# Optimization experiments

Measured on AMD Instinct MI355X. Metric: run time of the kernel, lower is better.

Reference implementation:

```python
import jax, jax.numpy as jnp
import numpy as np

N_NODES = 50000
N_EDGES = 800000
IN_F = 128
HID = 16
HEADS = 8
OUT_F = 128


def setup_inputs() -> dict:
    key = jax.random.key(0)
    ks = jax.random.split(key, 16)
    h = jax.random.normal(ks[0], (N_NODES, IN_F), dtype=jnp.float32)
    src1 = jax.random.randint(ks[1], (N_EDGES,), 0, N_NODES, dtype=jnp.int32)
    dst1 = jax.random.randint(ks[2], (N_EDGES,), 0, N_NODES, dtype=jnp.int32)
    src2 = jax.random.randint(ks[3], (N_EDGES,), 0, N_NODES, dtype=jnp.int32)
    dst2 = jax.random.randint(ks[4], (N_EDGES,), 0, N_NODES, dtype=jnp.int32)
    norm1 = jax.random.uniform(ks[5], (N_NODES, 1), dtype=jnp.float32)
    norm2 = jax.random.uniform(ks[6], (N_NODES, 1), dtype=jnp.float32)
    D = HEADS * HID  # 128
    W_lin = jax.random.normal(ks[7], (IN_F, D), dtype=jnp.float32) * (1.0 / np.sqrt(IN_F))
    b_lin = jax.random.normal(ks[8], (D,), dtype=jnp.float32) * 0.01
    al = jax.random.normal(ks[9], (HEADS, HID, 1), dtype=jnp.float32) * 0.1
    ar = jax.random.normal(ks[10], (HEADS, HID, 1), dtype=jnp.float32) * 0.1
    W_fc = jax.random.normal(ks[11], (D, OUT_F), dtype=jnp.float32) * (1.0 / np.sqrt(D))
    b_fc = jax.random.normal(ks[12], (OUT_F,), dtype=jnp.float32) * 0.01
    return {"h": h, "src1": src1, "dst1": dst1, "src2": src2, "dst2": dst2,
            "norm1": norm1, "norm2": norm2, "W_lin": W_lin, "b_lin": b_lin,
            "al": al, "ar": ar, "W_fc": W_fc, "b_fc": b_fc}


def _propagate(feat, norm, src, dst, n_nodes):
    # msg = h[src] * norm[src]; accum[v] = sum_{e: dst=v} msg_e; out = accum * norm
    msg = feat[src] * norm[src]                      # [E, D]
    agg = jax.ops.segment_sum(msg, dst, num_segments=n_nodes)
    return agg * norm                                # [N, D]


def _leaky_relu(x):
    return jnp.where(x > 0, x, 0.2 * x)


def reference(h, src1, dst1, src2, dst2, norm1, norm2, W_lin, b_lin, al, ar, W_fc, b_fc):
    N = h.shape[0]
    hf = h @ W_lin + b_lin                           # [N, 8*HID] (dropout p given but eval-mode -> identity)
    h1 = _propagate(hf, norm1, src1, dst1, N)
    h2 = _propagate(hf, norm2, src2, dst2, N)
    # Faithful to torch: row-major reshape [N, 8*HID] -> (8, N, HID)
    h1r = h1.reshape(HEADS, N, HID)
    h2r = h2.reshape(HEADS, N, HID)
    hr = hf.reshape(HEADS, N, HID)
    ai = jnp.einsum('hnd,hdo->hno', hr, al)          # [8, N, 1]
    aj1 = jnp.einsum('hnd,hdo->hno', h1r, ar)
    aj2 = jnp.einsum('hnd,hdo->hno', h2r, ar)
    a1 = jnp.clip(jnp.exp(_leaky_relu(ai + aj1)), -10.0, 10.0)
    a2 = jnp.clip(jnp.exp(_leaky_relu(ai + aj2)), -10.0, 10.0)
    denom = a1 + a2
    out = (a1 / denom) * h1r + (a2 / denom) * h2r    # [8, N, HID]
    out = out.reshape(N, HEADS * HID)
    return out @ W_fc + b_fc
```

## Files before the change

### kernel.cpp

```cpp
#include <hip/hip_runtime.h>

#define NN 50000
#define NE 800000
#define NB 196
#define NBLK 128
#define CHUNK 6250
#define MAXB 6144

typedef __bf16 bf16x8 __attribute__((ext_vector_type(8)));
typedef float  f32x4  __attribute__((ext_vector_type(4)));

__device__ __forceinline__ unsigned short f2bf(float x) {
    unsigned u = __float_as_uint(x);
    return (unsigned short)((u + 0x7FFFu + ((u >> 16) & 1u)) >> 16);
}
__device__ __forceinline__ float bflo(unsigned u) { return __uint_as_float(u << 16); }
__device__ __forceinline__ float bfhi(unsigned u) { return __uint_as_float(u & 0xFFFF0000u); }

__global__ __launch_bounds__(256) void convert_w_kernel(
    const float* __restrict__ Wa, const float* __restrict__ Wb,
    unsigned short* __restrict__ Wta, unsigned short* __restrict__ Wtb)
{
    __shared__ float ls[128 * 132];
    const float* W = blockIdx.x ? Wb : Wa;
    unsigned short* Wt = blockIdx.x ? Wtb : Wta;
    const int t = threadIdx.x;
    for (int i = t; i < 128 * 32; i += 256) {
        int k = i >> 5, n4 = i & 31;
        *(float4*)&ls[k * 132 + n4 * 4] = ((const float4*)W)[i];
    }
    __syncthreads();
    for (int j = t; j < 128 * 128; j += 256) {
        int n = j >> 7, k = j & 127;
        Wt[j] = f2bf(ls[k * 132 + n]);
    }
}

__global__ __launch_bounds__(256) void mfma_gemm_kernel(
    const float* __restrict__ X, const unsigned short* __restrict__ Wt,
    const float* __restrict__ bias, float* __restrict__ Y,
    unsigned short* __restrict__ Ybf, int nrows)
{
    __shared__ unsigned short Wl[128 * 128];
    const int t = threadIdx.x;
    const int lane = t & 63;
    const int wv = t >> 6;
    const int row0 = blockIdx.x * 64;
    const int m16 = lane & 15;
    const int quad = lane >> 4;

    {
        const uint4* Wg = (const uint4*)Wt;
        #pragma unroll
        for (int i = 0; i < 8; i++) {
            int gi = t + i * 256;
            int n = gi >> 4, g = gi & 15;
            uint4 v = Wg[gi];
            *(uint4*)&Wl[n * 128 + (((g ^ (n & 15)) << 3))] = v;
        }
    }

    const int arow = row0 + wv * 16 + m16;
    const bool valid = (arow < nrows);
    const float4* X4 = (const float4*)X;
    float4 xr[8];
    #pragma unroll
    for (int kc = 0; kc < 4; kc++) {
        if (valid) {
            int gidx = arow * 32 + kc * 8 + quad * 2;
            xr[kc * 2]     = X4[gidx];
            xr[kc * 2 + 1] = X4[gidx + 1];
        } else {
            xr[kc * 2] = xr[kc * 2 + 1] = make_float4(0.f, 0.f, 0.f, 0.f);
        }
    }
    __syncthreads();

    f32x4 acc[8];
    #pragma unroll
    for (int nt = 0; nt < 8; nt++) acc[nt] = (f32x4){0.f, 0.f, 0.f, 0.f};

    #pragma unroll
    for (int kc = 0; kc < 4; kc++) {
        union { unsigned short u[8]; bf16x8 v; } ah, al;
        float f[8] = { xr[kc*2].x, xr[kc*2].y, xr[kc*2].z, xr[kc*2].w,
                       xr[kc*2+1].x, xr[kc*2+1].y, xr[kc*2+1].z, xr[kc*2+1].w };
        #pragma unroll
        for (int j = 0; j < 8; j++) {
            unsigned u = __float_as_uint(f[j]);
            ah.u[j] = (unsigned short)(u >> 16);
            al.u[j] = f2bf(f[j] - __uint_as_float(u & 0xFFFF0000u));
        }
        const int sgbase = (kc * 4 + quad);
        #pragma unroll
        for (int nt = 0; nt < 8; nt++) {
            const int n = nt * 16 + m16;
            bf16x8 b = *(const bf16x8*)&Wl[n * 128 + ((sgbase ^ m16) << 3)];
            acc[nt] = __builtin_amdgcn_mfma_f32_16x16x32_bf16(ah.v, b, acc[nt], 0, 0, 0);
            acc[nt] = __builtin_amdgcn_mfma_f32_16x16x32_bf16(al.v, b, acc[nt], 0, 0, 0);
        }
    }

    #pragma unroll
    for (int nt = 0; nt < 8; nt++) {
        const int col = nt * 16 + m16;
        const float bc = bias[col];
        #pragma unroll
        for (int r = 0; r < 4; r++) {
            int row = row0 + wv * 16 + quad * 4 + r;
            if (row < nrows) {
                float val = acc[nt][r] + bc;
                if (Y)   Y[(long)row * 128 + col] = val;
                if (Ybf) Ybf[(long)row * 128 + col] = f2bf(val);
            }
        }
    }
}

__global__ __launch_bounds__(256) void mfma_gemm_bf16_kernel(
    const unsigned short* __restrict__ Xbf, const unsigned short* __restrict__ Wt,
    const float* __restrict__ bias, float* __restrict__ Y, int nrows)
{
    __shared__ unsigned short Wl[128 * 128];
    const int t = threadIdx.x;
    const int lane = t & 63;
    const int wv = t >> 6;
    const int row0 = blockIdx.x * 64;
    const int m16 = lane & 15;
    const int quad = lane >> 4;

    {
        const uint4* Wg = (const uint4*)Wt;
        #pragma unroll
        for (int i = 0; i < 8; i++) {
            int gi = t + i * 256;
            int n = gi >> 4, g = gi & 15;
            uint4 v = Wg[gi];
            *(uint4*)&Wl[n * 128 + (((g ^ (n & 15)) << 3))] = v;
        }
    }

    const int arow = row0 + wv * 16 + m16;
    const bool valid = (arow < nrows);
    const uint4* X16 = (const uint4*)Xbf;
    union { uint4 u; bf16x8 v; } xr[4];
    #pragma unroll
    for (int kc = 0; kc < 4; kc++) {
        if (valid) xr[kc].u = X16[arow * 16 + kc * 4 + quad];
        else       xr[kc].u = make_uint4(0, 0, 0, 0);
    }
    __syncthreads();

    f32x4 acc[8];
    #pragma unroll
    for (int nt = 0; nt < 8; nt++) acc[nt] = (f32x4){0.f, 0.f, 0.f, 0.f};

    #pragma unroll
    for (int kc = 0; kc < 4; kc++) {
        const int sgbase = (kc * 4 + quad);
        #pragma unroll
        for (int nt = 0; nt < 8; nt++) {
            const int n = nt * 16 + m16;
            bf16x8 b = *(const bf16x8*)&Wl[n * 128 + ((sgbase ^ m16) << 3)];
            acc[nt] = __builtin_amdgcn_mfma_f32_16x16x32_bf16(xr[kc].v, b, acc[nt], 0, 0, 0);
        }
    }

    #pragma unroll
    for (int nt = 0; nt < 8; nt++) {
        const int col = nt * 16 + m16;
        const float bc = bias[col];
        #pragma unroll
        for (int r = 0; r < 4; r++) {
            int row = row0 + wv * 16 + quad * 4 + r;
            if (row < nrows) Y[(long)row * 128 + col] = acc[nt][r] + bc;
        }
    }
}

__global__ __launch_bounds__(1024) void histA_kernel(
    const int* __restrict__ dst1, const int* __restrict__ dst2, int* __restrict__ histG)
{
    __shared__ int h[2 * NB];
    const int t = threadIdx.x, blk = blockIdx.x;
    for (int i = t; i < 2 * NB; i += 1024) h[i] = 0;
    __syncthreads();
    const int base = blk * CHUNK;
    for (int i = t; i < CHUNK; i += 1024) {
        atomicAdd(&h[dst1[base + i] >> 8], 1);
        atomicAdd(&h[NB + (dst2[base + i] >> 8)], 1);
    }
    __syncthreads();
    for (int i = t; i < 2 * NB; i += 1024)
        histG[(size_t)i * NBLK + blk] = h[i];
}

__global__ __launch_bounds__(NBLK) void scanB1_kernel(int* __restrict__ histG, int* __restrict__ btot)
{
    __shared__ int s[NBLK];
    const int t = threadIdx.x, row = blockIdx.x;
    int v = histG[(size_t)row * NBLK + t];
    s[t] = v;
    __syncthreads();
    for (int off = 1; off < NBLK; off <<= 1) {
        int x = (t >= off) ? s[t - off] : 0;
        __syncthreads();
        s[t] += x;
        __syncthreads();
    }
    histG[(size_t)row * NBLK + t] = s[t] - v;
    if (t == NBLK - 1) btot[row] = s[t];
}

__global__ __launch_bounds__(256) void scanB2_kernel(const int* __restrict__ btot, int* __restrict__ bbase)
{
    __shared__ int sc[256];
    const int t = threadIdx.x;
    for (int g = 0; g < 2; g++) {
        int v = (t < NB) ? btot[g * NB + t] : 0;
        sc[t] = v;
        __syncthreads();
        for (int off = 1; off < 256; off <<= 1) {
            int x = (t >= off) ? sc[t - off] : 0;
            __syncthreads();
            sc[t] += x;
            __syncthreads();
        }
        if (t < NB) bbase[g * NB + t] = sc[t] - v;
        __syncthreads();
    }
}

__global__ __launch_bounds__(1024) void scatterC_kernel(
    const int* __restrict__ src1, const int* __restrict__ dst1,
    const int* __restrict__ src2, const int* __restrict__ dst2,
    const int* __restrict__ histG, const int* __restrict__ bbase,
    unsigned int* __restrict__ bin1, unsigned int* __restrict__ bin2)
{
    __shared__ int pos[2 * NB];
    const int t = threadIdx.x, blk = blockIdx.x;
    for (int i = t; i < 2 * NB; i += 1024)
        pos[i] = bbase[i] + histG[(size_t)i * NBLK + blk];
    __syncthreads();
    const int base = blk * CHUNK;
    for (int i = t; i < CHUNK; i += 1024) {
        int d = dst1[base + i], s = src1[base + i];
        int slot = atomicAdd(&pos[d >> 8], 1);
        bin1[slot] = ((unsigned)(d & 255) << 16) | (unsigned)s;
        d = dst2[base + i]; s = src2[base + i];
        slot = atomicAdd(&pos[NB + (d >> 8)], 1);
        bin2[slot] = ((unsigned)(d & 255) << 16) | (unsigned)s;
    }
}

__global__ __launch_bounds__(256) void bucket_sort_kernel(
    const unsigned int* __restrict__ bin1, const unsigned int* __restrict__ bin2,
    const int* __restrict__ bbase, const int* __restrict__ btot,
    unsigned short* __restrict__ csr1, int* __restrict__ start1, int* __restrict__ deg1,
    unsigned short* __restrict__ csr2, int* __restrict__ start2, int* __restrict__ deg2)
{
    __shared__ int lcnt[256];
    __shared__ int sc[256];
    __shared__ int oat[256];
    __shared__ unsigned short outb[MAXB];
    const int t = threadIdx.x;
    const int g = (blockIdx.x >= NB) ? 1 : 0;
    const int b = blockIdx.x - g * NB;
    const unsigned int* bin = g ? bin2 : bin1;
    unsigned short* csr = g ? csr2 : csr1;
    int* start = g ? start2 : start1;
    int* deg   = g ? deg2 : deg1;

    const int base = bbase[g * NB + b];
    const int tot = min(btot[g * NB + b], MAXB);

    lcnt[t] = 0;
    __syncthreads();
    for (int i = t; i < tot; i += 256) atomicAdd(&lcnt[bin[base + i] >> 16], 1);
    __syncthreads();
    sc[t] = lcnt[t];
    __syncthreads();
    for (int off = 1; off < 256; off <<= 1) {
        int x = (t >= off) ? sc[t - off] : 0;
        __syncthreads();
        sc[t] += x;
        __syncthreads();
    }
    const int ex = sc[t] - lcnt[t];
    oat[t] = ex;
    __syncthreads();
    for (int i = t; i < tot; i += 256) {
        unsigned v = bin[base + i];
        int slot = atomicAdd(&oat[v >> 16], 1);
        outb[slot] = (unsigned short)(v & 0xFFFFu);
    }
    __syncthreads();
    for (int i = t; i < tot; i += 256) csr[base + i] = outb[i];
    int nd = b * 256 + t;
    if (nd < NN) { start[nd] = base + ex; deg[nd] = lcnt[t]; }
}

__global__ __launch_bounds__(256) void gather_attn_kernel(
    const unsigned int* __restrict__ hfb,
    const unsigned short* __restrict__ csr1, const int* __restrict__ start1,
    const int* __restrict__ deg1, const float* __restrict__ norm1,
    const unsigned short* __restrict__ csr2, const int* __restrict__ start2,
    const int* __restrict__ deg2, const float* __restrict__ norm2,
    const float* __restrict__ al, const float* __restrict__ ar,
    unsigned int* __restrict__ outb)
{
    const int lane = threadIdx.x & 63;
    int node = (blockIdx.x * 256 + threadIdx.x) >> 6;
    if (node >= NN) return;
    node = __builtin_amdgcn_readfirstlane(node);

    float2 acc1 = make_float2(0.f, 0.f), acc2 = make_float2(0.f, 0.f);

    #pragma unroll 1
    for (int g = 0; g < 2; g++) {
        const unsigned short* csr = g ? csr2 : csr1;
        const int* startp = g ? start2 : start1;
        const int* degp   = g ? deg2 : deg1;
        const float* norm = g ? norm2 : norm1;
        float2 acc = make_float2(0.f, 0.f);
        const int st = startp[node], dg = degp[node];
        for (int base = 0; base < dg; base += 64) {
            const int nb = min(64, dg - base);
            int myc = (lane < nb) ? (int)csr[st + base + lane] : 0;
            int j = 0;
            for (; j + 8 <= nb; j += 8) {
                int s[8]; float n[8]; unsigned u[8];
                #pragma unroll
                for (int q = 0; q < 8; q++) s[q] = __builtin_amdgcn_readlane(myc, j + q);
                #pragma unroll
                for (int q = 0; q < 8; q++) {
                    n[q] = norm[s[q]];
                    u[q] = hfb[(long)s[q] * 64 + lane];
                }
                #pragma unroll
                for (int q = 0; q < 8; q++) {
                    acc.x = fmaf(bflo(u[q]), n[q], acc.x);
                    acc.y = fmaf(bfhi(u[q]), n[q], acc.y);
                }
            }
            for (; j < nb; j++) {
                int s = __builtin_amdgcn_readlane(myc, j);
                float nv = norm[s];
                unsigned u = hfb[(long)s * 64 + lane];
                acc.x = fmaf(bflo(u), nv, acc.x);
                acc.y = fmaf(bfhi(u), nv, acc.y);
            }
        }
        if (g) acc2 = acc; else acc1 = acc;
    }

    const float nn1 = norm1[node], nn2 = norm2[node];
    acc1.x *= nn1; acc1.y *= nn1;
    acc2.x *= nn2; acc2.y *= nn2;

    const int cc = lane >> 3;
    const int m = node * 8 + cc;
    const int head = m / NN;
    const int hid = (2 * lane) & 15;
    unsigned uf = hfb[(long)node * 64 + lane];
    const float fx = bflo(uf), fy = bfhi(uf);
    const float av0 = al[head * 16 + hid], av1 = al[head * 16 + hid + 1];
    const float rv0 = ar[head * 16 + hid], rv1 = ar[head * 16 + hid + 1];
    float s_ai = fx * av0 + fy * av1;
    float s1 = acc1.x * rv0 + acc1.y * rv1;
    float s2 = acc2.x * rv0 + acc2.y * rv1;
    s_ai += __shfl_xor(s_ai, 1); s_ai += __shfl_xor(s_ai, 2); s_ai += __shfl_xor(s_ai, 4);
    s1   += __shfl_xor(s1, 1);   s1   += __shfl_xor(s1, 2);   s1   += __shfl_xor(s1, 4);
    s2   += __shfl_xor(s2, 1);   s2   += __shfl_xor(s2, 2);   s2   += __shfl_xor(s2, 4);
    float x1 = s_ai + s1; x1 = x1 > 0.f ? x1 : 0.2f * x1;
    float x2 = s_ai + s2; x2 = x2 > 0.f ? x2 : 0.2f * x2;
    float e1 = fminf(expf(x1), 10.f);
    float e2 = fminf(expf(x2), 10.f);
    float inv = 1.f / (e1 + e2);
    float w1 = e1 * inv, w2 = e2 * inv;
    float ox = w1 * acc1.x + w2 * acc2.x;
    float oy = w1 * acc1.y + w2 * acc2.y;
    outb[(long)node * 64 + lane] = (unsigned)f2bf(ox) | ((unsigned)f2bf(oy) << 16);
}

extern "C" void kernel_launch(void* const* d_in, const int* in_sizes, int n_in,
                              void* d_out, int out_size, void* d_ws, size_t ws_size,
                              hipStream_t stream)
{
    const float* h     = (const float*)d_in[0];
    const int*   src1  = (const int*)  d_in[1];
    const int*   dst1  = (const int*)  d_in[2];
    const int*   src2  = (const int*)  d_in[3];
    const int*   dst2  = (const int*)  d_in[4];
    const float* norm1 = (const float*)d_in[5];
    const float* norm2 = (const float*)d_in[6];
    const float* W_lin = (const float*)d_in[7];
    const float* b_lin = (const float*)d_in[8];
    const float* al    = (const float*)d_in[9];
    const float* ar    = (const float*)d_in[10];
    const float* W_fc  = (const float*)d_in[11];
    const float* b_fc  = (const float*)d_in[12];
    float* out = (float*)d_out;

    unsigned short* hfb  = (unsigned short*)d_ws;
    unsigned short* outbf = hfb + (size_t)NN * 128;
    unsigned int* bin1 = (unsigned int*)(outbf + (size_t)NN * 128);
    unsigned int* bin2 = bin1 + NE;
    unsigned short* csr1 = (unsigned short*)(bin2 + NE);
    unsigned short* csr2 = csr1 + NE;
    unsigned short* WtL  = csr2 + NE;
    unsigned short* WtF  = WtL + 128 * 128;
    int* histG  = (int*)(WtF + 128 * 128);
    int* btot   = histG + 2 * NB * NBLK;
    int* bbase  = btot + 2 * NB;
    int* start1 = bbase + 2 * NB;
    int* start2 = start1 + NN;
    int* deg1   = start2 + NN;
    int* deg2   = deg1 + NN;

    convert_w_kernel<<<2, 256, 0, stream>>>(W_lin, W_fc, WtL, WtF);

    mfma_gemm_kernel<<<(NN + 63) / 64, 256, 0, stream>>>(h, WtL, b_lin, nullptr, hfb, NN);

    histA_kernel<<<NBLK, 1024, 0, stream>>>(dst1, dst2, histG);
    scanB1_kernel<<<2 * NB, NBLK, 0, stream>>>(histG, btot);
    scanB2_kernel<<<1, 256, 0, stream>>>(btot, bbase);
    scatterC_kernel<<<NBLK, 1024, 0, stream>>>(src1, dst1, src2, dst2, histG, bbase, bin1, bin2);
    bucket_sort_kernel<<<2 * NB, 256, 0, stream>>>(bin1, bin2, bbase, btot,
                                                   csr1, start1, deg1,
                                                   csr2, start2, deg2);

    gather_attn_kernel<<<(NN * 64 + 255) / 256, 256, 0, stream>>>(
        (const unsigned int*)hfb,
        csr1, start1, deg1, norm1,
        csr2, start2, deg2, norm2,
        al, ar, (unsigned int*)outbf);

    mfma_gemm_bf16_kernel<<<(NN + 63) / 64, 256, 0, stream>>>(outbf, WtF, b_fc, out, NN);
}
```

Measured before the change: 227.7 us.

## Fuse CSR build into one cooperative kernel and gather two edges per wave

Merges weight conversion, histogram, the two scans, the scatter and the bucket sort into a single cooperative kernel of 512 blocks separated by grid syncs. This removes five kernel launches and the gaps between them. The gather kernel now processes two edges per wave iteration, each half-wave loading 8 bytes per lane, and combines the halves with a cross-half shuffle. The grid syncs add barrier cost, and the cooperative launch requires all 512 blocks to be resident at once.

```diff
diff --git a/kernel.cpp b/kernel.cpp
--- a/kernel.cpp
+++ b/kernel.cpp
@@ -1,10 +1,13 @@
 #include <hip/hip_runtime.h>
+#include <hip/hip_cooperative_groups.h>
+
+namespace cg = cooperative_groups;
 
 #define NN 50000
 #define NE 800000
 #define NB 196
-#define NBLK 128
-#define CHUNK 6250
+#define NBLK 512
+#define CHUNK 1563
 #define MAXB 6144
 
 typedef __bf16 bf16x8 __attribute__((ext_vector_type(8)));
@@ -17,22 +20,138 @@
 __device__ __forceinline__ float bflo(unsigned u) { return __uint_as_float(u << 16); }
 __device__ __forceinline__ float bfhi(unsigned u) { return __uint_as_float(u & 0xFFFF0000u); }
 
-__global__ __launch_bounds__(256) void convert_w_kernel(
+struct SortSM { int lcnt[256]; int sc[256]; int oat[256]; unsigned short outb[MAXB]; };
+
+__global__ __launch_bounds__(256, 2) void build_kernel(
     const float* __restrict__ Wa, const float* __restrict__ Wb,
-    unsigned short* __restrict__ Wta, unsigned short* __restrict__ Wtb)
+    unsigned short* __restrict__ Wta, unsigned short* __restrict__ Wtb,
+    const int* __restrict__ src1, const int* __restrict__ dst1,
+    const int* __restrict__ src2, const int* __restrict__ dst2,
+    int* __restrict__ histG, int* __restrict__ btot, int* __restrict__ bbase,
+    unsigned int* __restrict__ bin1, unsigned int* __restrict__ bin2,
+    unsigned short* __restrict__ csr1, int* __restrict__ start1, int* __restrict__ deg1,
+    unsigned short* __restrict__ csr2, int* __restrict__ start2, int* __restrict__ deg2)
 {
-    __shared__ float ls[128 * 132];
-    const float* W = blockIdx.x ? Wb : Wa;
-    unsigned short* Wt = blockIdx.x ? Wtb : Wta;
+    __shared__ union {
+        int h[2 * NB];
+        int s[256];
+        int pos[2 * NB];
+        SortSM srt;
+    } sm;
+    cg::grid_group grid = cg::this_grid();
     const int t = threadIdx.x;
-    for (int i = t; i < 128 * 32; i += 256) {
-        int k = i >> 5, n4 = i & 31;
-        *(float4*)&ls[k * 132 + n4 * 4] = ((const float4*)W)[i];
-    }
-    __syncthreads();
-    for (int j = t; j < 128 * 128; j += 256) {
-        int n = j >> 7, k = j & 127;
-        Wt[j] = f2bf(ls[k * 132 + n]);
+    const int blk = blockIdx.x;
+
+    {
+        for (int i = t; i < 2 * NB; i += 256) sm.h[i] = 0;
+        __syncthreads();
+        const int base = blk * CHUNK;
+        const int lim = min(CHUNK, NE - base);
+        for (int i = t; i < lim; i += 256) {
+            atomicAdd(&sm.h[dst1[base + i] >> 8], 1);
+            atomicAdd(&sm.h[NB + (dst2[base + i] >> 8)], 1);
+        }
+        __syncthreads();
+        for (int i = t; i < 2 * NB; i += 256)
+            histG[(size_t)i * NBLK + blk] = sm.h[i];
+        if (blk < 2) {
+            const float* W = blk ? Wb : Wa;
+            unsigned short* Wt = blk ? Wtb : Wta;
+            for (int j = t; j < 128 * 128; j += 256) {
+                int n = j >> 7, k = j & 127;
+                Wt[j] = f2bf(W[k * 128 + n]);
+            }
+        }
+    }
+    grid.sync();
+
+    if (blk < 2 * NB) {
+        int* rowp = histG + (size_t)blk * NBLK;
+        int v0 = rowp[2 * t], v1 = rowp[2 * t + 1];
+        sm.s[t] = v0 + v1;
+        __syncthreads();
+        for (int off = 1; off < 256; off <<= 1) {
+            int x = (t >= off) ? sm.s[t - off] : 0;
+            __syncthreads();
+            sm.s[t] += x;
+            __syncthreads();
+        }
+        int incl = sm.s[t];
+        int e0 = incl - (v0 + v1);
+        rowp[2 * t] = e0;
+        rowp[2 * t + 1] = e0 + v0;
+        if (t == 255) btot[blk] = incl;
+    }
+    grid.sync();
+
+    if (blk == 0) {
+        for (int g = 0; g < 2; g++) {
+            int v = (t < NB) ? btot[g * NB + t] : 0;
+            sm.s[t] = v;
+            __syncthreads();
+            for (int off = 1; off < 256; off <<= 1) {
+                int x = (t >= off) ? sm.s[t - off] : 0;
+                __syncthreads();
+                sm.s[t] += x;
+                __syncthreads();
+            }
+            if (t < NB) bbase[g * NB + t] = sm.s[t] - v;
+            __syncthreads();
+        }
+    }
+    grid.sync();
+
+    {
+        for (int i = t; i < 2 * NB; i += 256)
+            sm.pos[i] = bbase[i] + histG[(size_t)i * NBLK + blk];
+        __syncthreads();
+        const int base = blk * CHUNK;
+        const int lim = min(CHUNK, NE - base);
+        for (int i = t; i < lim; i += 256) {
+            int d = dst1[base + i], s = src1[base + i];
+            int slot = atomicAdd(&sm.pos[d >> 8], 1);
+            bin1[slot] = ((unsigned)(d & 255) << 16) | (unsigned)s;
+            d = dst2[base + i]; s = src2[base + i];
+            slot = atomicAdd(&sm.pos[NB + (d >> 8)], 1);
+            bin2[slot] = ((unsigned)(d & 255) << 16) | (unsigned)s;
+        }
+    }
+    grid.sync();
+
+    if (blk < 2 * NB) {
+        const int g = (blk >= NB) ? 1 : 0;
+        const int b = blk - g * NB;
+        const unsigned int* bin = g ? bin2 : bin1;
+        unsigned short* csr = g ? csr2 : csr1;
+        int* start = g ? start2 : start1;
+        int* deg   = g ? deg2 : deg1;
+        const int base = bbase[g * NB + b];
+        const int tot = min(btot[g * NB + b], MAXB);
+
+        sm.srt.lcnt[t] = 0;
+        __syncthreads();
+        for (int i = t; i < tot; i += 256) atomicAdd(&sm.srt.lcnt[bin[base + i] >> 16], 1);
+        __syncthreads();
+        sm.srt.sc[t] = sm.srt.lcnt[t];
+        __syncthreads();
+        for (int off = 1; off < 256; off <<= 1) {
+            int x = (t >= off) ? sm.srt.sc[t - off] : 0;
+            __syncthreads();
+            sm.srt.sc[t] += x;
+            __syncthreads();
+        }
+        const int ex = sm.srt.sc[t] - sm.srt.lcnt[t];
+        sm.srt.oat[t] = ex;
+        __syncthreads();
+        for (int i = t; i < tot; i += 256) {
+            unsigned v = bin[base + i];
+            int slot = atomicAdd(&sm.srt.oat[v >> 16], 1);
+            sm.srt.outb[slot] = (unsigned short)(v & 0xFFFFu);
+        }
+        __syncthreads();
+        for (int i = t; i < tot; i += 256) csr[base + i] = sm.srt.outb[i];
+        int nd = b * 256 + t;
+        if (nd < NN) { start[nd] = base + ex; deg[nd] = sm.srt.lcnt[t]; }
     }
 }
 
@@ -178,128 +297,6 @@
     }
 }
 
-__global__ __launch_bounds__(1024) void histA_kernel(
-    const int* __restrict__ dst1, const int* __restrict__ dst2, int* __restrict__ histG)
-{
-    __shared__ int h[2 * NB];
-    const int t = threadIdx.x, blk = blockIdx.x;
-    for (int i = t; i < 2 * NB; i += 1024) h[i] = 0;
-    __syncthreads();
-    const int base = blk * CHUNK;
-    for (int i = t; i < CHUNK; i += 1024) {
-        atomicAdd(&h[dst1[base + i] >> 8], 1);
-        atomicAdd(&h[NB + (dst2[base + i] >> 8)], 1);
-    }
-    __syncthreads();
-    for (int i = t; i < 2 * NB; i += 1024)
-        histG[(size_t)i * NBLK + blk] = h[i];
-}
-
-__global__ __launch_bounds__(NBLK) void scanB1_kernel(int* __restrict__ histG, int* __restrict__ btot)
-{
-    __shared__ int s[NBLK];
-    const int t = threadIdx.x, row = blockIdx.x;
-    int v = histG[(size_t)row * NBLK + t];
-    s[t] = v;
-    __syncthreads();
-    for (int off = 1; off < NBLK; off <<= 1) {
-        int x = (t >= off) ? s[t - off] : 0;
-        __syncthreads();
-        s[t] += x;
-        __syncthreads();
-    }
-    histG[(size_t)row * NBLK + t] = s[t] - v;
-    if (t == NBLK - 1) btot[row] = s[t];
-}
-
-__global__ __launch_bounds__(256) void scanB2_kernel(const int* __restrict__ btot, int* __restrict__ bbase)
-{
-    __shared__ int sc[256];
-    const int t = threadIdx.x;
-    for (int g = 0; g < 2; g++) {
-        int v = (t < NB) ? btot[g * NB + t] : 0;
-        sc[t] = v;
-        __syncthreads();
-        for (int off = 1; off < 256; off <<= 1) {
-            int x = (t >= off) ? sc[t - off] : 0;
-            __syncthreads();
-            sc[t] += x;
-            __syncthreads();
-        }
-        if (t < NB) bbase[g * NB + t] = sc[t] - v;
-        __syncthreads();
-    }
-}
-
-__global__ __launch_bounds__(1024) void scatterC_kernel(
-    const int* __restrict__ src1, const int* __restrict__ dst1,
-    const int* __restrict__ src2, const int* __restrict__ dst2,
-    const int* __restrict__ histG, const int* __restrict__ bbase,
-    unsigned int* __restrict__ bin1, unsigned int* __restrict__ bin2)
-{
-    __shared__ int pos[2 * NB];
-    const int t = threadIdx.x, blk = blockIdx.x;
-    for (int i = t; i < 2 * NB; i += 1024)
-        pos[i] = bbase[i] + histG[(size_t)i * NBLK + blk];
-    __syncthreads();
-    const int base = blk * CHUNK;
-    for (int i = t; i < CHUNK; i += 1024) {
-        int d = dst1[base + i], s = src1[base + i];
-        int slot = atomicAdd(&pos[d >> 8], 1);
-        bin1[slot] = ((unsigned)(d & 255) << 16) | (unsigned)s;
-        d = dst2[base + i]; s = src2[base + i];
-        slot = atomicAdd(&pos[NB + (d >> 8)], 1);
-        bin2[slot] = ((unsigned)(d & 255) << 16) | (unsigned)s;
-    }
-}
-
-__global__ __launch_bounds__(256) void bucket_sort_kernel(
-    const unsigned int* __restrict__ bin1, const unsigned int* __restrict__ bin2,
-    const int* __restrict__ bbase, const int* __restrict__ btot,
-    unsigned short* __restrict__ csr1, int* __restrict__ start1, int* __restrict__ deg1,
-    unsigned short* __restrict__ csr2, int* __restrict__ start2, int* __restrict__ deg2)
-{
-    __shared__ int lcnt[256];
-    __shared__ int sc[256];
-    __shared__ int oat[256];
-    __shared__ unsigned short outb[MAXB];
-    const int t = threadIdx.x;
-    const int g = (blockIdx.x >= NB) ? 1 : 0;
-    const int b = blockIdx.x - g * NB;
-    const unsigned int* bin = g ? bin2 : bin1;
-    unsigned short* csr = g ? csr2 : csr1;
-    int* start = g ? start2 : start1;
-    int* deg   = g ? deg2 : deg1;
-
-    const int base = bbase[g * NB + b];
-    const int tot = min(btot[g * NB + b], MAXB);
-
-    lcnt[t] = 0;
-    __syncthreads();
-    for (int i = t; i < tot; i += 256) atomicAdd(&lcnt[bin[base + i] >> 16], 1);
-    __syncthreads();
-    sc[t] = lcnt[t];
-    __syncthreads();
-    for (int off = 1; off < 256; off <<= 1) {
-        int x = (t >= off) ? sc[t - off] : 0;
-        __syncthreads();
-        sc[t] += x;
-        __syncthreads();
-    }
-    const int ex = sc[t] - lcnt[t];
-    oat[t] = ex;
-    __syncthreads();
-    for (int i = t; i < tot; i += 256) {
-        unsigned v = bin[base + i];
-        int slot = atomicAdd(&oat[v >> 16], 1);
-        outb[slot] = (unsigned short)(v & 0xFFFFu);
-    }
-    __syncthreads();
-    for (int i = t; i < tot; i += 256) csr[base + i] = outb[i];
-    int nd = b * 256 + t;
-    if (nd < NN) { start[nd] = base + ex; deg[nd] = lcnt[t]; }
-}
-
 __global__ __launch_bounds__(256) void gather_attn_kernel(
     const unsigned int* __restrict__ hfb,
     const unsigned short* __restrict__ csr1, const int* __restrict__ start1,
@@ -310,11 +307,14 @@
     unsigned int* __restrict__ outb)
 {
     const int lane = threadIdx.x & 63;
+    const int half = lane & 31;
+    const bool hi = (lane & 32) != 0;
     int node = (blockIdx.x * 256 + threadIdx.x) >> 6;
     if (node >= NN) return;
     node = __builtin_amdgcn_readfirstlane(node);
 
-    float2 acc1 = make_float2(0.f, 0.f), acc2 = make_float2(0.f, 0.f);
+    float4 acc1 = make_float4(0.f, 0.f, 0.f, 0.f);
+    float4 acc2 = make_float4(0.f, 0.f, 0.f, 0.f);
 
     #pragma unroll 1
     for (int g = 0; g < 2; g++) {
@@ -322,65 +322,96 @@
         const int* startp = g ? start2 : start1;
         const int* degp   = g ? deg2 : deg1;
         const float* norm = g ? norm2 : norm1;
-        float2 acc = make_float2(0.f, 0.f);
+        float4 acc = make_float4(0.f, 0.f, 0.f, 0.f);
         const int st = startp[node], dg = degp[node];
         for (int base = 0; base < dg; base += 64) {
             const int nb = min(64, dg - base);
             int myc = (lane < nb) ? (int)csr[st + base + lane] : 0;
+            const int npairs = nb >> 1;
             int j = 0;
-            for (; j + 8 <= nb; j += 8) {
-                int s[8]; float n[8]; unsigned u[8];
+            for (; j + 4 <= npairs; j += 4) {
+                float fn[4]; uint2 u[4];
                 #pragma unroll
-                for (int q = 0; q < 8; q++) s[q] = __builtin_amdgcn_readlane(myc, j + q);
-                #pragma unroll
-                for (int q = 0; q < 8; q++) {
-                    n[q] = norm[s[q]];
-                    u[q] = hfb[(long)s[q] * 64 + lane];
+                for (int p = 0; p < 4; p++) {
+                    int e = (j + p) * 2;
+                    int s0 = __builtin_amdgcn_readlane(myc, e);
+                    int s1 = __builtin_amdgcn_readlane(myc, e + 1);
+                    float n0 = norm[s0], n1 = norm[s1];
+                    int ss = hi ? s1 : s0;
+                    fn[p] = hi ? n1 : n0;
+                    u[p] = *(const uint2*)(hfb + ss * 64 + half * 2);
                 }
                 #pragma unroll
-                for (int q = 0; q < 8; q++) {
-                    acc.x = fmaf(bflo(u[q]), n[q], acc.x);
-                    acc.y = fmaf(bfhi(u[q]), n[q], acc.y);
+                for (int p = 0; p < 4; p++) {
+                    acc.x = fmaf(bflo(u[p].x), fn[p], acc.x);
+                    acc.y = fmaf(bfhi(u[p].x), fn[p], acc.y);
+                    acc.z = fmaf(bflo(u[p].y), fn[p], acc.z);
+                    acc.w = fmaf(bfhi(u[p].y), fn[p], acc.w);
                 }
             }
-            for (; j < nb; j++) {
-                int s = __builtin_amdgcn_readlane(myc, j);
-                float nv = norm[s];
-                unsigned u = hfb[(long)s * 64 + lane];
-                acc.x = fmaf(bflo(u), nv, acc.x);
-                acc.y = fmaf(bfhi(u), nv, acc.y);
-            }
-        }
+            for (; j < npairs; j++) {
+                int e = j * 2;
+                int s0 = __builtin_amdgcn_readlane(myc, e);
+                int s1 = __builtin_amdgcn_readlane(myc, e + 1);
+                float n0 = norm[s0], n1 = norm[s1];
+                int ss = hi ? s1 : s0;
+                float fn = hi ? n1 : n0;
+                uint2 u = *(const uint2*)(hfb + ss * 64 + half * 2);
+                acc.x = fmaf(bflo(u.x), fn, acc.x);
+                acc.y = fmaf(bfhi(u.x), fn, acc.y);
+                acc.z = fmaf(bflo(u.y), fn, acc.z);
+                acc.w = fmaf(bfhi(u.y), fn, acc.w);
+            }
+            if (nb & 1) {
+                int s0 = __builtin_amdgcn_readlane(myc, nb - 1);
+                float fn = hi ? 0.f : norm[s0];
+                uint2 u = *(const uint2*)(hfb + s0 * 64 + half * 2);
+                acc.x = fmaf(bflo(u.x), fn, acc.x);
+                acc.y = fmaf(bfhi(u.x), fn, acc.y);
+                acc.z = fmaf(bflo(u.y), fn, acc.z);
+                acc.w = fmaf(bfhi(u.y), fn, acc.w);
+            }
+        }
+        acc.x += __shfl_xor(acc.x, 32);
+        acc.y += __shfl_xor(acc.y, 32);
+        acc.z += __shfl_xor(acc.z, 32);
+        acc.w += __shfl_xor(acc.w, 32);
         if (g) acc2 = acc; else acc1 = acc;
     }
 
     const float nn1 = norm1[node], nn2 = norm2[node];
-    acc1.x *= nn1; acc1.y *= nn1;
-    acc2.x *= nn2; acc2.y *= nn2;
-
-    const int cc = lane >> 3;
+    acc1.x *= nn1; acc1.y *= nn1; acc1.z *= nn1; acc1.w *= nn1;
+    acc2.x *= nn2; acc2.y *= nn2; acc2.z *= nn2; acc2.w *= nn2;
+
+    const int cc = half >> 2;
     const int m = node * 8 + cc;
     const int head = m / NN;
-    const int hid = (2 * lane) & 15;
-    unsigned uf = hfb[(long)node * 64 + lane];
-    const float fx = bflo(uf), fy = bfhi(uf);
-    const float av0 = al[head * 16 + hid], av1 = al[head * 16 + hid + 1];
-    const float rv0 = ar[head * 16 + hid], rv1 = ar[head * 16 + hid + 1];
-    float s_ai = fx * av0 + fy * av1;
-    float s1 = acc1.x * rv0 + acc1.y * rv1;
-    float s2 = acc2.x * rv0 + acc2.y * rv1;
-    s_ai += __shfl_xor(s_ai, 1); s_ai += __shfl_xor(s_ai, 2); s_ai += __shfl_xor(s_ai, 4);
-    s1   += __shfl_xor(s1, 1);   s1   += __shfl_xor(s1, 2);   s1   += __shfl_xor(s1, 4);
-    s2   += __shfl_xor(s2, 1);   s2   += __shfl_xor(s2, 2);   s2   += __shfl_xor(s2, 4);
+    const int hid = (half & 3) * 4;
+    uint2 uf = *(const uint2*)(hfb + node * 64 + half * 2);
+    float4 f = make_float4(bflo(uf.x), bfhi(uf.x), bflo(uf.y), bfhi(uf.y));
+    float4 av = *(const float4*)&al[head * 16 + hid];
+    float4 rv = *(const float4*)&ar[head * 16 + hid];
+    float s_ai = f.x * av.x + f.y * av.y + f.z * av.z + f.w * av.w;
+    float s1 = acc1.x * rv.x + acc1.y * rv.y + acc1.z * rv.z + acc1.w * rv.w;
+    float s2 = acc2.x * rv.x + acc2.y * rv.y + acc2.z * rv.z + acc2.w * rv.w;
+    s_ai += __shfl_xor(s_ai, 1); s_ai += __shfl_xor(s_ai, 2);
+    s1   += __shfl_xor(s1, 1);   s1   += __shfl_xor(s1, 2);
+    s2   += __shfl_xor(s2, 1);   s2   += __shfl_xor(s2, 2);
     float x1 = s_ai + s1; x1 = x1 > 0.f ? x1 : 0.2f * x1;
     float x2 = s_ai + s2; x2 = x2 > 0.f ? x2 : 0.2f * x2;
     float e1 = fminf(expf(x1), 10.f);
     float e2 = fminf(expf(x2), 10.f);
     float inv = 1.f / (e1 + e2);
     float w1 = e1 * inv, w2 = e2 * inv;
-    float ox = w1 * acc1.x + w2 * acc2.x;
-    float oy = w1 * acc1.y + w2 * acc2.y;
-    outb[(long)node * 64 + lane] = (unsigned)f2bf(ox) | ((unsigned)f2bf(oy) << 16);
+    float o0 = w1 * acc1.x + w2 * acc2.x;
+    float o1 = w1 * acc1.y + w2 * acc2.y;
+    float o2 = w1 * acc1.z + w2 * acc2.z;
+    float o3 = w1 * acc1.w + w2 * acc2.w;
+    if (lane < 32) {
+        unsigned p0 = (unsigned)f2bf(o0) | ((unsigned)f2bf(o1) << 16);
+        unsigned p1 = (unsigned)f2bf(o2) | ((unsigned)f2bf(o3) << 16);
+        ((uint2*)outb)[node * 32 + half] = make_uint2(p0, p1);
+    }
 }
 
 extern "C" void kernel_launch(void* const* d_in, const int* in_sizes, int n_in,
@@ -418,19 +449,22 @@
     int* deg1   = start2 + NN;
     int* deg2   = deg1 + NN;
 
-    convert_w_kernel<<<2, 256, 0, stream>>>(W_lin, W_fc, WtL, WtF);
+    {
+        void* args[] = {
+            (void*)&W_lin, (void*)&W_fc, (void*)&WtL, (void*)&WtF,
+            (void*)&src1, (void*)&dst1, (void*)&src2, (void*)&dst2,
+            (void*)&histG, (void*)&btot, (void*)&bbase,
+            (void*)&bin1, (void*)&bin2,
+            (void*)&csr1, (void*)&start1, (void*)&deg1,
+            (void*)&csr2, (void*)&start2, (void*)&deg2
+        };
+        hipLaunchCooperativeKernel((void*)build_kernel, dim3(NBLK), dim3(256),
+                                   args, 0, stream);
+    }
 
     mfma_gemm_kernel<<<(NN + 63) / 64, 256, 0, stream>>>(h, WtL, b_lin, nullptr, hfb, NN);
 
-    histA_kernel<<<NBLK, 1024, 0, stream>>>(dst1, dst2, histG);
-    scanB1_kernel<<<2 * NB, NBLK, 0, stream>>>(histG, btot);
-    scanB2_kernel<<<1, 256, 0, stream>>>(btot, bbase);
-    scatterC_kernel<<<NBLK, 1024, 0, stream>>>(src1, dst1, src2, dst2, histG, bbase, bin1, bin2);
-    bucket_sort_kernel<<<2 * NB, 256, 0, stream>>>(bin1, bin2, bbase, btot,
-                                                   csr1, start1, deg1,
-                                                   csr2, start2, deg2);
-
-    gather_attn_kernel<<<(NN * 64 + 255) / 256, 256, 0, stream>>>(
+    gather_attn_kernel<<<(NN * 64) / 256, 256, 0, stream>>>(
         (const unsigned int*)hfb,
         csr1, start1, deg1, norm1,
         csr2, start2, deg2, norm2,
```

New measurement: 479.5 us. 111% more time.

## Fold weight conversion into histogram kernel and merge scans into scatter

Applied to the files above, without the earlier changes.

Weight transposition/bf16 conversion now runs as two extra blocks of the histogram kernel instead of a separate launch. The two scan kernels are removed: each scatter block recomputes the per-bucket totals and its own prefix across all histogram chunks, then does a block-wide scan to get the bucket bases, with block 0 writing bbase/btot for the later sort. The histogram layout is transposed to chunk-major. This removes three kernel launches and their serialization, at the cost of every scatter block redundantly reading the full 128x392 histogram and doing an extra LDS scan.

```diff
diff --git a/kernel.cpp b/kernel.cpp
--- a/kernel.cpp
+++ b/kernel.cpp
@@ -3,6 +3,7 @@
 #define NN 50000
 #define NE 800000
 #define NB 196
+#define NBG 392
 #define NBLK 128
 #define CHUNK 6250
 #define MAXB 6144
@@ -17,173 +18,23 @@
 __device__ __forceinline__ float bflo(unsigned u) { return __uint_as_float(u << 16); }
 __device__ __forceinline__ float bfhi(unsigned u) { return __uint_as_float(u & 0xFFFF0000u); }
 
-__global__ __launch_bounds__(256) void convert_w_kernel(
+__global__ __launch_bounds__(1024) void histA_kernel(
+    const int* __restrict__ dst1, const int* __restrict__ dst2, int* __restrict__ histG,
     const float* __restrict__ Wa, const float* __restrict__ Wb,
     unsigned short* __restrict__ Wta, unsigned short* __restrict__ Wtb)
 {
-    __shared__ float ls[128 * 132];
-    const float* W = blockIdx.x ? Wb : Wa;
-    unsigned short* Wt = blockIdx.x ? Wtb : Wta;
-    const int t = threadIdx.x;
-    for (int i = t; i < 128 * 32; i += 256) {
-        int k = i >> 5, n4 = i & 31;
-        *(float4*)&ls[k * 132 + n4 * 4] = ((const float4*)W)[i];
-    }
-    __syncthreads();
-    for (int j = t; j < 128 * 128; j += 256) {
-        int n = j >> 7, k = j & 127;
-        Wt[j] = f2bf(ls[k * 132 + n]);
-    }
-}
-
-__global__ __launch_bounds__(256) void mfma_gemm_kernel(
-    const float* __restrict__ X, const unsigned short* __restrict__ Wt,
-    const float* __restrict__ bias, float* __restrict__ Y,
-    unsigned short* __restrict__ Ybf, int nrows)
-{
-    __shared__ unsigned short Wl[128 * 128];
-    const int t = threadIdx.x;
-    const int lane = t & 63;
-    const int wv = t >> 6;
-    const int row0 = blockIdx.x * 64;
-    const int m16 = lane & 15;
-    const int quad = lane >> 4;
-
-    {
-        const uint4* Wg = (const uint4*)Wt;
-        #pragma unroll
-        for (int i = 0; i < 8; i++) {
-            int gi = t + i * 256;
-            int n = gi >> 4, g = gi & 15;
-            uint4 v = Wg[gi];
-            *(uint4*)&Wl[n * 128 + (((g ^ (n & 15)) << 3))] = v;
-        }
-    }
-
-    const int arow = row0 + wv * 16 + m16;
-    const bool valid = (arow < nrows);
-    const float4* X4 = (const float4*)X;
-    float4 xr[8];
-    #pragma unroll
-    for (int kc = 0; kc < 4; kc++) {
-        if (valid) {
-            int gidx = arow * 32 + kc * 8 + quad * 2;
-            xr[kc * 2]     = X4[gidx];
-            xr[kc * 2 + 1] = X4[gidx + 1];
-        } else {
-            xr[kc * 2] = xr[kc * 2 + 1] = make_float4(0.f, 0.f, 0.f, 0.f);
-        }
-    }
-    __syncthreads();
-
-    f32x4 acc[8];
-    #pragma unroll
-    for (int nt = 0; nt < 8; nt++) acc[nt] = (f32x4){0.f, 0.f, 0.f, 0.f};
-
-    #pragma unroll
-    for (int kc = 0; kc < 4; kc++) {
-        union { unsigned short u[8]; bf16x8 v; } ah, al;
-        float f[8] = { xr[kc*2].x, xr[kc*2].y, xr[kc*2].z, xr[kc*2].w,
-                       xr[kc*2+1].x, xr[kc*2+1].y, xr[kc*2+1].z, xr[kc*2+1].w };
-        #pragma unroll
-        for (int j = 0; j < 8; j++) {
-            unsigned u = __float_as_uint(f[j]);
-            ah.u[j] = (unsigned short)(u >> 16);
-            al.u[j] = f2bf(f[j] - __uint_as_float(u & 0xFFFF0000u));
-        }
-        const int sgbase = (kc * 4 + quad);
-        #pragma unroll
-        for (int nt = 0; nt < 8; nt++) {
-            const int n = nt * 16 + m16;
-            bf16x8 b = *(const bf16x8*)&Wl[n * 128 + ((sgbase ^ m16) << 3)];
-            acc[nt] = __builtin_amdgcn_mfma_f32_16x16x32_bf16(ah.v, b, acc[nt], 0, 0, 0);
-            acc[nt] = __builtin_amdgcn_mfma_f32_16x16x32_bf16(al.v, b, acc[nt], 0, 0, 0);
-        }
-    }
-
-    #pragma unroll
-    for (int nt = 0; nt < 8; nt++) {
-        const int col = nt * 16 + m16;
-        const float bc = bias[col];
-        #pragma unroll
-        for (int r = 0; r < 4; r++) {
-            int row = row0 + wv * 16 + quad * 4 + r;
-            if (row < nrows) {
-                float val = acc[nt][r] + bc;
-                if (Y)   Y[(long)row * 128 + col] = val;
-                if (Ybf) Ybf[(long)row * 128 + col] = f2bf(val);
-            }
-        }
-    }
-}
-
-__global__ __launch_bounds__(256) void mfma_gemm_bf16_kernel(
-    const unsigned short* __restrict__ Xbf, const unsigned short* __restrict__ Wt,
-    const float* __restrict__ bias, float* __restrict__ Y, int nrows)
-{
-    __shared__ unsigned short Wl[128 * 128];
-    const int t = threadIdx.x;
-    const int lane = t & 63;
-    const int wv = t >> 6;
-    const int row0 = blockIdx.x * 64;
-    const int m16 = lane & 15;
-    const int quad = lane >> 4;
-
-    {
-        const uint4* Wg = (const uint4*)Wt;
-        #pragma unroll
-        for (int i = 0; i < 8; i++) {
-            int gi = t + i * 256;
-            int n = gi >> 4, g = gi & 15;
-            uint4 v = Wg[gi];
-            *(uint4*)&Wl[n * 128 + (((g ^ (n & 15)) << 3))] = v;
-        }
-    }
-
-    const int arow = row0 + wv * 16 + m16;
-    const bool valid = (arow < nrows);
-    const uint4* X16 = (const uint4*)Xbf;
-    union { uint4 u; bf16x8 v; } xr[4];
-    #pragma unroll
-    for (int kc = 0; kc < 4; kc++) {
-        if (valid) xr[kc].u = X16[arow * 16 + kc * 4 + quad];
-        else       xr[kc].u = make_uint4(0, 0, 0, 0);
-    }
-    __syncthreads();
-
-    f32x4 acc[8];
-    #pragma unroll
-    for (int nt = 0; nt < 8; nt++) acc[nt] = (f32x4){0.f, 0.f, 0.f, 0.f};
-
-    #pragma unroll
-    for (int kc = 0; kc < 4; kc++) {
-        const int sgbase = (kc * 4 + quad);
-        #pragma unroll
-        for (int nt = 0; nt < 8; nt++) {
-            const int n = nt * 16 + m16;
-            bf16x8 b = *(const bf16x8*)&Wl[n * 128 + ((sgbase ^ m16) << 3)];
-            acc[nt] = __builtin_amdgcn_mfma_f32_16x16x32_bf16(xr[kc].v, b, acc[nt], 0, 0, 0);
-        }
-    }
-
-    #pragma unroll
-    for (int nt = 0; nt < 8; nt++) {
-        const int col = nt * 16 + m16;
-        const float bc = bias[col];
-        #pragma unroll
-        for (int r = 0; r < 4; r++) {
-            int row = row0 + wv * 16 + quad * 4 + r;
-            if (row < nrows) Y[(long)row * 128 + col] = acc[nt][r] + bc;
-        }
-    }
-}
-
-__global__ __launch_bounds__(1024) void histA_kernel(
-    const int* __restrict__ dst1, const int* __restrict__ dst2, int* __restrict__ histG)
-{
-    __shared__ int h[2 * NB];
     const int t = threadIdx.x, blk = blockIdx.x;
-    for (int i = t; i < 2 * NB; i += 1024) h[i] = 0;
+    if (blk >= NBLK) {
+        const float* W = (blk - NBLK) ? Wb : Wa;
+        unsigned short* Wt = (blk - NBLK) ? Wtb : Wta;
+        for (int j = t; j < 128 * 128; j += 1024) {
+            int n = j >> 7, k = j & 127;
+            Wt[j] = f2bf(W[k * 128 + n]);
+        }
+        return;
+    }
+    __shared__ int h[NBG];
+    for (int i = t; i < NBG; i += 1024) h[i] = 0;
     __syncthreads();
     const int base = blk * CHUNK;
     for (int i = t; i < CHUNK; i += 1024) {
@@ -191,65 +42,55 @@
         atomicAdd(&h[NB + (dst2[base + i] >> 8)], 1);
     }
     __syncthreads();
-    for (int i = t; i < 2 * NB; i += 1024)
-        histG[(size_t)i * NBLK + blk] = h[i];
-}
-
-__global__ __launch_bounds__(NBLK) void scanB1_kernel(int* __restrict__ histG, int* __restrict__ btot)
-{
-    __shared__ int s[NBLK];
-    const int t = threadIdx.x, row = blockIdx.x;
-    int v = histG[(size_t)row * NBLK + t];
-    s[t] = v;
-    __syncthreads();
-    for (int off = 1; off < NBLK; off <<= 1) {
-        int x = (t >= off) ? s[t - off] : 0;
-        __syncthreads();
-        s[t] += x;
-        __syncthreads();
-    }
-    histG[(size_t)row * NBLK + t] = s[t] - v;
-    if (t == NBLK - 1) btot[row] = s[t];
-}
-
-__global__ __launch_bounds__(256) void scanB2_kernel(const int* __restrict__ btot, int* __restrict__ bbase)
-{
-    __shared__ int sc[256];
-    const int t = threadIdx.x;
-    for (int g = 0; g < 2; g++) {
-        int v = (t < NB) ? btot[g * NB + t] : 0;
-        sc[t] = v;
-        __syncthreads();
-        for (int off = 1; off < 256; off <<= 1) {
-            int x = (t >= off) ? sc[t - off] : 0;
-            __syncthreads();
-            sc[t] += x;
-            __syncthreads();
-        }
-        if (t < NB) bbase[g * NB + t] = sc[t] - v;
-        __syncthreads();
-    }
+    for (int i = t; i < NBG; i += 1024)
+        histG[blk * NBG + i] = h[i];
 }
 
 __global__ __launch_bounds__(1024) void scatterC_kernel(
     const int* __restrict__ src1, const int* __restrict__ dst1,
     const int* __restrict__ src2, const int* __restrict__ dst2,
-    const int* __restrict__ histG, const int* __restrict__ bbase,
+    const int* __restrict__ histG,
+    int* __restrict__ gbbase, int* __restrict__ gbtot,
     unsigned int* __restrict__ bin1, unsigned int* __restrict__ bin2)
 {
-    __shared__ int pos[2 * NB];
+    __shared__ int s[512];
+    __shared__ int pos[NBG];
     const int t = threadIdx.x, blk = blockIdx.x;
-    for (int i = t; i < 2 * NB; i += 1024)
-        pos[i] = bbase[i] + histG[(size_t)i * NBLK + blk];
-    __syncthreads();
+
+    int total_i = 0, pref_i = 0;
+    if (t < NBG) {
+        for (int c = 0; c < NBLK; c++) {
+            int v = histG[c * NBG + t];
+            total_i += v;
+            if (c < blk) pref_i += v;
+        }
+    }
+    if (t < 512) s[t] = (t < NBG) ? total_i : 0;
+    __syncthreads();
+    for (int off = 1; off < 512; off <<= 1) {
+        int x = 0;
+        if (t < 512 && t >= off) x = s[t - off];
+        __syncthreads();
+        if (t < 512) s[t] += x;
+        __syncthreads();
+    }
+    const int sumG1 = s[NB - 1];
+    if (t < NBG) {
+        int excl = s[t] - total_i;
+        int bb = excl - ((t >= NB) ? sumG1 : 0);
+        pos[t] = bb + pref_i;
+        if (blk == 0) { gbbase[t] = bb; gbtot[t] = total_i; }
+    }
+    __syncthreads();
+
     const int base = blk * CHUNK;
     for (int i = t; i < CHUNK; i += 1024) {
-        int d = dst1[base + i], s = src1[base + i];
+        int d = dst1[base + i], sv = src1[base + i];
         int slot = atomicAdd(&pos[d >> 8], 1);
-        bin1[slot] = ((unsigned)(d & 255) << 16) | (unsigned)s;
-        d = dst2[base + i]; s = src2[base + i];
+        bin1[slot] = ((unsigned)(d & 255) << 16) | (unsigned)sv;
+        d = dst2[base + i]; sv = src2[base + i];
         slot = atomicAdd(&pos[NB + (d >> 8)], 1);
-        bin2[slot] = ((unsigned)(d & 255) << 16) | (unsigned)s;
+        bin2[slot] = ((unsigned)(d & 255) << 16) | (unsigned)sv;
     }
 }
 
@@ -298,6 +139,148 @@
     for (int i = t; i < tot; i += 256) csr[base + i] = outb[i];
     int nd = b * 256 + t;
     if (nd < NN) { start[nd] = base + ex; deg[nd] = lcnt[t]; }
+}
+
+__global__ __launch_bounds__(256) void mfma_gemm_kernel(
+    const float* __restrict__ X, const unsigned short* __restrict__ Wt,
+    const float* __restrict__ bias, float* __restrict__ Y,
+    unsigned short* __restrict__ Ybf, int nrows)
+{
+    __shared__ unsigned short Wl[128 * 128];
+    const int t = threadIdx.x;
+    const int lane = t & 63;
+    const int wv = t >> 6;
+    const int row0 = blockIdx.x * 64;
+    const int m16 = lane & 15;
+    const int quad = lane >> 4;
+
+    {
+        const uint4* Wg = (const uint4*)Wt;
+        #pragma unroll
+        for (int i = 0; i < 8; i++) {
+            int gi = t + i * 256;
+            int n = gi >> 4, g = gi & 15;
+            uint4 v = Wg[gi];
+            *(uint4*)&Wl[n * 128 + (((g ^ (n & 15)) << 3))] = v;
+        }
+    }
+
+    const int arow = row0 + wv * 16 + m16;
+    const bool valid = (arow < nrows);
+    const float4* X4 = (const float4*)X;
+    float4 xr[8];
+    #pragma unroll
+    for (int kc = 0; kc < 4; kc++) {
+        if (valid) {
+            int gidx = arow * 32 + kc * 8 + quad * 2;
+            xr[kc * 2]     = X4[gidx];
+            xr[kc * 2 + 1] = X4[gidx + 1];
+        } else {
+            xr[kc * 2] = xr[kc * 2 + 1] = make_float4(0.f, 0.f, 0.f, 0.f);
+        }
+    }
+    __syncthreads();
+
+    f32x4 acc[8];
+    #pragma unroll
+    for (int nt = 0; nt < 8; nt++) acc[nt] = (f32x4){0.f, 0.f, 0.f, 0.f};
+
+    #pragma unroll
+    for (int kc = 0; kc < 4; kc++) {
+        union { unsigned short u[8]; bf16x8 v; } ah, al;
+        float f[8] = { xr[kc*2].x, xr[kc*2].y, xr[kc*2].z, xr[kc*2].w,
+                       xr[kc*2+1].x, xr[kc*2+1].y, xr[kc*2+1].z, xr[kc*2+1].w };
+        #pragma unroll
+        for (int j = 0; j < 8; j++) {
+            unsigned u = __float_as_uint(f[j]);
+            ah.u[j] = (unsigned short)(u >> 16);
+            al.u[j] = f2bf(f[j] - __uint_as_float(u & 0xFFFF0000u));
+        }
+        const int sgbase = (kc * 4 + quad);
+        #pragma unroll
+        for (int nt = 0; nt < 8; nt++) {
+            const int n = nt * 16 + m16;
+            bf16x8 b = *(const bf16x8*)&Wl[n * 128 + ((sgbase ^ m16) << 3)];
+            acc[nt] = __builtin_amdgcn_mfma_f32_16x16x32_bf16(ah.v, b, acc[nt], 0, 0, 0);
+            acc[nt] = __builtin_amdgcn_mfma_f32_16x16x32_bf16(al.v, b, acc[nt], 0, 0, 0);
+        }
+    }
+
+    #pragma unroll
+    for (int nt = 0; nt < 8; nt++) {
+        const int col = nt * 16 + m16;
+        const float bc = bias[col];
+        #pragma unroll
+        for (int r = 0; r < 4; r++) {
+            int row = row0 + wv * 16 + quad * 4 + r;
+            if (row < nrows) {
+                float val = acc[nt][r] + bc;
+                if (Y)   Y[(long)row * 128 + col] = val;
+                if (Ybf) Ybf[(long)row * 128 + col] = f2bf(val);
+            }
+        }
+    }
+}
+
+__global__ __launch_bounds__(256) void mfma_gemm_bf16_kernel(
+    const unsigned short* __restrict__ Xbf, const unsigned short* __restrict__ Wt,
+    const float* __restrict__ bias, float* __restrict__ Y, int nrows)
+{
+    __shared__ unsigned short Wl[128 * 128];
+    const int t = threadIdx.x;
+    const int lane = t & 63;
+    const int wv = t >> 6;
+    const int row0 = blockIdx.x * 64;
+    const int m16 = lane & 15;
+    const int quad = lane >> 4;
+
+    {
+        const uint4* Wg = (const uint4*)Wt;
+        #pragma unroll
+        for (int i = 0; i < 8; i++) {
+            int gi = t + i * 256;
+            int n = gi >> 4, g = gi & 15;
+            uint4 v = Wg[gi];
+            *(uint4*)&Wl[n * 128 + (((g ^ (n & 15)) << 3))] = v;
+        }
+    }
+
+    const int arow = row0 + wv * 16 + m16;
+    const bool valid = (arow < nrows);
+    const uint4* X16 = (const uint4*)Xbf;
+    union { uint4 u; bf16x8 v; } xr[4];
+    #pragma unroll
+    for (int kc = 0; kc < 4; kc++) {
+        if (valid) xr[kc].u = X16[arow * 16 + kc * 4 + quad];
+        else       xr[kc].u = make_uint4(0, 0, 0, 0);
+    }
+    __syncthreads();
+
+    f32x4 acc[8];
+    #pragma unroll
+    for (int nt = 0; nt < 8; nt++) acc[nt] = (f32x4){0.f, 0.f, 0.f, 0.f};
+
+    #pragma unroll
+    for (int kc = 0; kc < 4; kc++) {
+        const int sgbase = (kc * 4 + quad);
+        #pragma unroll
+        for (int nt = 0; nt < 8; nt++) {
+            const int n = nt * 16 + m16;
+            bf16x8 b = *(const bf16x8*)&Wl[n * 128 + ((sgbase ^ m16) << 3)];
+            acc[nt] = __builtin_amdgcn_mfma_f32_16x16x32_bf16(xr[kc].v, b, acc[nt], 0, 0, 0);
+        }
+    }
+
+    #pragma unroll
+    for (int nt = 0; nt < 8; nt++) {
+        const int col = nt * 16 + m16;
+        const float bc = bias[col];
+        #pragma unroll
+        for (int r = 0; r < 4; r++) {
+            int row = row0 + wv * 16 + quad * 4 + r;
+            if (row < nrows) Y[(long)row * 128 + col] = acc[nt][r] + bc;
+        }
+    }
 }
 
 __global__ __launch_bounds__(256) void gather_attn_kernel(
@@ -411,26 +394,25 @@
     unsigned short* WtL  = csr2 + NE;
     unsigned short* WtF  = WtL + 128 * 128;
     int* histG  = (int*)(WtF + 128 * 128);
-    int* btot   = histG + 2 * NB * NBLK;
-    int* bbase  = btot + 2 * NB;
-    int* start1 = bbase + 2 * NB;
+    int* btot   = histG + NBLK * NBG;
+    int* bbase  = btot + NBG;
+    int* start1 = bbase + NBG;
     int* start2 = start1 + NN;
     int* deg1   = start2 + NN;
     int* deg2   = deg1 + NN;
 
-    convert_w_kernel<<<2, 256, 0, stream>>>(W_lin, W_fc, WtL, WtF);
+    histA_kernel<<<NBLK + 2, 1024, 0, stream>>>(dst1, dst2, histG, W_lin, W_fc, WtL, WtF);
 
     mfma_gemm_kernel<<<(NN + 63) / 64, 256, 0, stream>>>(h, WtL, b_lin, nullptr, hfb, NN);
 
-    histA_kernel<<<NBLK, 1024, 0, stream>>>(dst1, dst2, histG);
-    scanB1_kernel<<<2 * NB, NBLK, 0, stream>>>(histG, btot);
-    scanB2_kernel<<<1, 256, 0, stream>>>(btot, bbase);
-    scatterC_kernel<<<NBLK, 1024, 0, stream>>>(src1, dst1, src2, dst2, histG, bbase, bin1, bin2);
-    bucket_sort_kernel<<<2 * NB, 256, 0, stream>>>(bin1, bin2, bbase, btot,
-                                                   csr1, start1, deg1,
-                                                   csr2, start2, deg2);
-
-    gather_attn_kernel<<<(NN * 64 + 255) / 256, 256, 0, stream>>>(
+    scatterC_kernel<<<NBLK, 1024, 0, stream>>>(src1, dst1, src2, dst2, histG,
+                                               bbase, btot, bin1, bin2);
+
+    bucket_sort_kernel<<<NBG, 256, 0, stream>>>(bin1, bin2, bbase, btot,
+                                                csr1, start1, deg1,
+                                                csr2, start2, deg2);
+
+    gather_attn_kernel<<<(NN * 64) / 256, 256, 0, stream>>>(
         (const unsigned int*)hfb,
         csr1, start1, deg1, norm1,
         csr2, start2, deg2, norm2,
```

After: 224.3 us. About the same (-1.5%).
